# Kernel tuning notes

Measured on AMD Instinct MI355X. Metric: run time of the kernel, lower is better.

Reference implementation:

```python
import jax, jax.numpy as jnp
import numpy as np

ACT_SCALE = 1.0 / 12.0
BATCH = 2_097_152
HIDDEN = 32


def _xavier(key, shape):
    fan_out, fan_in = shape
    std = (2.0 / (fan_in + fan_out)) ** 0.5
    return jax.random.normal(key, shape, dtype=jnp.float32) * std


def setup_inputs() -> dict:
    key = jax.random.key(0)
    ks = jax.random.split(key, 12)
    return {
        "eps_flat": jax.random.normal(ks[0], (BATCH, 3), dtype=jnp.float32) * 0.1,
        "B_first_w": _xavier(ks[1], (HIDDEN, 2)),
        "B_first_b": jax.random.normal(ks[2], (HIDDEN,), dtype=jnp.float32) * 0.05,
        "raw_A_0": jax.random.normal(ks[3], (HIDDEN, HIDDEN), dtype=jnp.float32) * 0.1,
        "raw_A_1": jax.random.normal(ks[4], (HIDDEN, HIDDEN), dtype=jnp.float32) * 0.1,
        "Bs_w_0": _xavier(ks[5], (HIDDEN, 2)),
        "Bs_b_0": jax.random.normal(ks[6], (HIDDEN,), dtype=jnp.float32) * 0.05,
        "Bs_w_1": _xavier(ks[7], (HIDDEN, 2)),
        "Bs_b_1": jax.random.normal(ks[8], (HIDDEN,), dtype=jnp.float32) * 0.05,
        "raw_A_out": jax.random.normal(ks[9], (1, HIDDEN), dtype=jnp.float32) * 0.1,
        "B_out_w": _xavier(ks[10], (1, 2)),
        "B_out_b": jax.random.normal(ks[11], (1,), dtype=jnp.float32) * 0.05,
    }


def reference(eps_flat, B_first_w, B_first_b, raw_A_0, raw_A_1,
              Bs_w_0, Bs_b_0, Bs_w_1, Bs_b_1, raw_A_out, B_out_w, B_out_b):
    sp = jax.nn.softplus

    def forward_W(z0):
        # z0: (n, 2) -> W: (n, 1). Dropout p=0 -> identity.
        z = sp(z0 @ B_first_w.T + B_first_b)
        for rawA, Bw, Bb in ((raw_A_0, Bs_w_0, Bs_b_0), (raw_A_1, Bs_w_1, Bs_b_1)):
            z = ACT_SCALE * sp(z @ sp(rawA).T) ** 2 + sp(z0 @ Bw.T + Bb)
        return z @ sp(raw_A_out).T + z0 @ B_out_w.T + B_out_b

    e11, e22, e12 = eps_flat[:, 0], eps_flat[:, 1], eps_flat[:, 2]
    I1 = e11 + e22
    I2 = e11 ** 2 + 2.0 * e12 ** 2 + e22 ** 2
    z0 = jnp.stack([I1, I2], axis=-1)  # (B, 2)

    W_sum = lambda z: forward_W(z).sum()
    grads = jax.grad(W_sum)(z0)                       # (B, 2) per-sample dW/dz0
    z0_ref = jnp.zeros((1, 2), dtype=eps_flat.dtype)
    dWdI1_ref = jax.grad(W_sum)(z0_ref)[0, 0]         # scalar reference correction

    dW_dI1 = grads[:, 0] - dWdI1_ref
    dW_dI2 = grads[:, 1]
    s11 = dW_dI1 + 2.0 * e11 * dW_dI2
    s22 = dW_dI1 + 2.0 * e22 * dW_dI2
    s12 = 2.0 * e12 * dW_dI2
    return jnp.stack([s11, s22, s12], axis=-1)
```

## Files before the change

kernel.cpp:

```cpp
#include <hip/hip_runtime.h>

typedef __attribute__((ext_vector_type(8)))  short s8b;
typedef __attribute__((ext_vector_type(16))) float f32x16;
typedef __attribute__((ext_vector_type(4)))  uint  uint4v;
typedef __attribute__((ext_vector_type(2)))  float float2v;
typedef __attribute__((ext_vector_type(4)))  float float4v;
typedef uint __attribute__((may_alias)) uint_ma;

static constexpr int   kBatch    = 2097152;
static constexpr float kActScale = 1.0f / 12.0f;
static constexpr float kAct2     = 1.0f / 6.0f;

__device__ float g_tab[40];
__device__ __attribute__((aligned(16))) ushort g_wt[4][2][2][64][8];

__device__ __forceinline__ float rcp_f(float x) { return __fdividef(1.0f, x); }
__device__ __forceinline__ float sp_only(float x) {
    float e = __expf(-fabsf(x));
    return fmaxf(x, 0.0f) + __logf(1.0f + e);
}
__device__ __forceinline__ float sig_only(float x) {
    float e = __expf(-fabsf(x));
    float r = rcp_f(1.0f + e);
    return (x >= 0.0f) ? r : e * r;
}
__device__ __forceinline__ float sp_sig(float x, float& sig) {
    float e  = __expf(-fabsf(x));
    float oe = 1.0f + e;
    float r  = rcp_f(oe);
    sig = (x >= 0.0f) ? r : e * r;
    return fmaxf(x, 0.0f) + __logf(oe);
}

__device__ __forceinline__ float log1p_e(float e) {
    return e * fmaf(e, fmaf(e, fmaf(e, fmaf(e, 0.03215845f, -0.13606275f),
                                    0.28947478f), -0.49190896f), 0.99949556f);
}
__device__ __forceinline__ float rcp12(float u) {
    float r = fmaf(u, -0.5f, 1.4571068f);
    r = r * fmaf(-u, r, 2.0f);
    r = r * fmaf(-u, r, 2.0f);
    return r;
}
__device__ __forceinline__ float sp_sig_p(float x, float& sig) {
    float e = __expf(-fabsf(x));
    float r = rcp12(1.0f + e);
    sig = (x >= 0.0f) ? r : e * r;
    return fmaxf(x, 0.0f) + log1p_e(e);
}
__device__ __forceinline__ float sp_sig_pos(float x, float& sig) {
    float e = __expf(-x);
    sig = rcp12(1.0f + e);
    return x + log1p_e(e);
}
__device__ __forceinline__ float sig_only_p(float x) {
    float e = __expf(-fabsf(x));
    float r = rcp12(1.0f + e);
    return (x >= 0.0f) ? r : e * r;
}

__device__ __forceinline__ uint  bf16u(float x) {
    uint u = __float_as_uint(x);
    return (u + 0x7FFFu + ((u >> 16) & 1u)) >> 16;
}
__device__ __forceinline__ float bf16f(uint h) { return __uint_as_float(h << 16); }
__device__ __forceinline__ uint cvt_pk_bf16(float lo, float hi) {
    uint r;
    asm("v_cvt_pk_bf16_f32 %0, %1, %2" : "=v"(r) : "v"(lo), "v"(hi));
    return r;
}
__device__ __forceinline__ void pswap(uint& a, uint& b) {
    asm("v_permlane32_swap_b32 %0, %1" : "+v"(a), "+v"(b));
}

__global__ __launch_bounds__(256) void icnn_prep(
    const float* __restrict__ rawA0, const float* __restrict__ rawA1,
    const float* __restrict__ rawAout,
    const float* __restrict__ W1,  const float* __restrict__ b1,
    const float* __restrict__ Wc0, const float* __restrict__ bc0,
    const float* __restrict__ Wc1, const float* __restrict__ bc1,
    const float* __restrict__ wout)
{
    __shared__ float sA0[1024], sA1[1024], sAout[32];
    const int t = threadIdx.x;
    for (int k = t; k < 1024; k += 256) sA0[k] = sp_only(rawA0[k]);
    for (int k = t; k < 1024; k += 256) sA1[k] = sp_only(rawA1[k]);
    if (t < 32) { float v = sp_only(rawAout[t]); sAout[t] = v; g_tab[t] = v; }
    __syncthreads();

    for (int k = t; k < 8192; k += 256) {
        int m = k >> 11, r = k & 2047;
        int hl = r >> 10, c = (r >> 9) & 1, l = (r >> 3) & 63, b = r & 7;
        int row = l & 31, j = 16 * c + 8 * (l >> 5) + b;
        float v;
        if      (m == 0) v = sA0[row * 32 + j];
        else if (m == 1) v = sA1[row * 32 + j];
        else if (m == 2) v = sA1[j * 32 + row];
        else             v = sA0[j * 32 + row];
        uint hi = bf16u(v);
        g_wt[m][hl][c][l][b] = (ushort)(hl == 0 ? hi : bf16u(v - bf16f(hi)));
    }

    if (t < 32) {
        const int i = t;
        float sa, sc0v;
        float zi = sp_sig(b1[i], sa);
        float u = 0.0f;
        for (int j = 0; j < 32; j++) u = fmaf(sA0[i * 32 + j], __shfl(zi, j, 64), u);
        float su; float t0 = sp_sig(u, su);
        float d0 = kAct2 * t0 * su;
        float spc = sp_sig(bc0[i], sc0v);
        float zn = fmaf(kActScale * t0, t0, spc);
        float u1 = 0.0f;
        for (int j = 0; j < 32; j++) u1 = fmaf(sA1[i * 32 + j], __shfl(zn, j, 64), u1);
        float su1; float t1 = sp_sig(u1, su1);
        float d1 = sAout[i] * kAct2 * t1 * su1;
        float contrib = Wc1[2 * i] * sAout[i] * sig_only(bc1[i]);
        float g = 0.0f;
        for (int j = 0; j < 32; j++) g = fmaf(sA1[j * 32 + i], __shfl(d1, j, 64), g);
        contrib = fmaf(Wc0[2 * i], g * sc0v, contrib);
        float gu0 = g * d0;
        float ga = 0.0f;
        for (int j = 0; j < 32; j++) ga = fmaf(sA0[j * 32 + i], __shfl(gu0, j, 64), ga);
        ga *= sa;
        contrib = fmaf(W1[2 * i], ga, contrib);
        for (int off = 16; off >= 1; off >>= 1)
            contrib += __shfl_down(contrib, off, 32);
        if (i == 0) g_tab[32] = wout[0] + contrib;
    }
}

__device__ __forceinline__ s8b ldwt(int m, int hl, int c, int lane) {
    const uint_ma* p = (const uint_ma*)&g_wt[m][hl][c][lane][0];
    uint4v q; q.x = p[0]; q.y = p[1]; q.z = p[2]; q.w = p[3];
    return __builtin_bit_cast(s8b, q);
}

#define OFF(e) (((e) & 3) + 8 * ((e) >> 2))

#define SWAPJ(PZ, FA, FB) { \
    uint s0 = PZ[0], s1 = PZ[1], s2 = PZ[2], s3 = PZ[3]; \
    uint s4 = PZ[4], s5 = PZ[5], s6 = PZ[6], s7 = PZ[7]; \
    pswap(s0, s2); pswap(s1, s3); pswap(s4, s6); pswap(s5, s7); \
    uint4v qa, qb; \
    qa.x = s0; qa.y = s1; qa.z = s2; qa.w = s3; \
    qb.x = s4; qb.y = s5; qb.z = s6; qb.w = s7; \
    FA = __builtin_bit_cast(s8b, qa); FB = __builtin_bit_cast(s8b, qb); }

#define MM(m, BA, BB, ACC) { \
    ACC = __builtin_amdgcn_mfma_f32_32x32x16_bf16(ldwt(m, 0, 0, lane), BA, ACC, 0, 0, 0); \
    ACC = __builtin_amdgcn_mfma_f32_32x32x16_bf16(ldwt(m, 0, 1, lane), BB, ACC, 0, 0, 0); \
    ACC = __builtin_amdgcn_mfma_f32_32x32x16_bf16(ldwt(m, 1, 0, lane), BA, ACC, 0, 0, 0); \
    ACC = __builtin_amdgcn_mfma_f32_32x32x16_bf16(ldwt(m, 1, 1, lane), BB, ACC, 0, 0, 0); }

__global__ __launch_bounds__(256) void icnn_main(
    const float* __restrict__ eps,
    const float* __restrict__ W1,  const float* __restrict__ b1,
    const float* __restrict__ Wc0, const float* __restrict__ bc0,
    const float* __restrict__ Wc1, const float* __restrict__ bc1,
    const float* __restrict__ wout,
    float* __restrict__ out)
{
    __shared__ uint carr[4][2][544];
    const int tid  = threadIdx.x;
    const int lane = tid & 63, wib = tid >> 6;
    const bool hb_ = lane >= 32;
    const int  hB  = hb_ ? 1 : 0;
    const int  rowl = lane & 31;
    const long rowg = ((long)blockIdx.x * 4 + wib) * 32 + rowl;
    uint* __restrict__ ca = &carr[wib][0][0];
    uint* __restrict__ cc = &carr[wib][1][0];

    const float e11 = eps[rowg * 3 + 0];
    const float e22 = eps[rowg * 3 + 1];
    const float e12 = eps[rowg * 3 + 2];
    const float x1 = e11 + e22;
    const float x2 = e11 * e11 + 2.0f * e12 * e12 + e22 * e22;

    const float wout0 = wout[0], wout1 = wout[1];
    const float cref  = g_tab[32];
    const char* W1c  = (const char*)W1;
    const char* b1c  = (const char*)b1;
    const char* Wc0c = (const char*)Wc0;
    const char* bc0c = (const char*)bc0;
    const char* Wc1c = (const char*)Wc1;
    const char* bc1c = (const char*)bc1;
    const char* aoc  = (const char*)&g_tab[0];

    float g0p = 0.0f, gqp = 0.0f;

    uint zf[2][4];
    #pragma unroll
    for (int c = 0; c < 2; ++c)
    #pragma unroll
    for (int s = 0; s < 4; ++s) {
        const float4v w4 = *(const float4v*)(W1c + 64 * hB + 128 * c + 16 * s);
        const float2v b2 = *(const float2v*)(b1c + 32 * hB + 64 * c + 8 * s);
        float a0 = fmaf(w4.x, x1, fmaf(w4.y, x2, b2.x));
        float a1 = fmaf(w4.z, x1, fmaf(w4.w, x2, b2.y));
        float s0, s1;
        float z0 = sp_sig_p(a0, s0);
        float z1 = sp_sig_p(a1, s1);
        zf[c][s] = cvt_pk_bf16(z0, z1);
        ca[rowl * 17 + 8 * c + 4 * hB + s] = cvt_pk_bf16(s0, s1);
    }
    uint4v zq0, zq1;
    zq0.x = zf[0][0]; zq0.y = zf[0][1]; zq0.z = zf[0][2]; zq0.w = zf[0][3];
    zq1.x = zf[1][0]; zq1.y = zf[1][1]; zq1.z = zf[1][2]; zq1.w = zf[1][3];
    s8b fA = __builtin_bit_cast(s8b, zq0);
    s8b fB = __builtin_bit_cast(s8b, zq1);

    f32x16 acc = {};
    MM(0, fA, fB, acc)

    uint pd0[8], pz[8];
    #pragma unroll
    for (int q = 0; q < 8; ++q) {
        const int e = 2 * q, off = OFF(e);
        const float4v wc = *(const float4v*)(Wc0c + 32 * hB + 8 * off);
        const float2v bc = *(const float2v*)(bc0c + 16 * hB + 4 * off);
        float su;  float t  = sp_sig_pos(acc[e], su);
        float su2; float t2 = sp_sig_pos(acc[e + 1], su2);
        float c0a = fmaf(wc.x, x1, fmaf(wc.y, x2, bc.x));
        float c0b = fmaf(wc.z, x1, fmaf(wc.w, x2, bc.y));
        float sc0, sc1;
        float spc0 = sp_sig_p(c0a, sc0);
        float spc1 = sp_sig_p(c0b, sc1);
        cc[rowl * 17 + 2 * hB + (off >> 1)] = cvt_pk_bf16(sc0, sc1);
        pd0[q] = cvt_pk_bf16(kAct2 * t * su, kAct2 * t2 * su2);
        pz[q]  = cvt_pk_bf16(fmaf(kActScale * t, t, spc0),
                             fmaf(kActScale * t2, t2, spc1));
    }
    SWAPJ(pz, fA, fB)

    f32x16 acc1 = {};
    MM(1, fA, fB, acc1)

    uint pdd[8];
    #pragma unroll
    for (int q = 0; q < 8; ++q) {
        const int e = 2 * q, off = OFF(e);
        const float4v wc = *(const float4v*)(Wc1c + 32 * hB + 8 * off);
        const float2v bc = *(const float2v*)(bc1c + 16 * hB + 4 * off);
        const float2v ao = *(const float2v*)(aoc  + 16 * hB + 4 * off);
        float c1a = fmaf(wc.x, x1, fmaf(wc.y, x2, bc.x));
        float c1b = fmaf(wc.z, x1, fmaf(wc.w, x2, bc.y));
        float wA = ao.x * sig_only_p(c1a);
        float wB = ao.y * sig_only_p(c1b);
        g0p = fmaf(wc.x, wA, g0p); gqp = fmaf(wc.y, wA, gqp);
        g0p = fmaf(wc.z, wB, g0p); gqp = fmaf(wc.w, wB, gqp);
        float su;  float t  = sp_sig_pos(acc1[e], su);
        float su2; float t2 = sp_sig_pos(acc1[e + 1], su2);
        pdd[q] = cvt_pk_bf16(ao.x * kAct2 * t * su, ao.y * kAct2 * t2 * su2);
    }
    SWAPJ(pdd, fA, fB)

    f32x16 acc2 = {};
    MM(2, fA, fB, acc2)

    uint pgg[8];
    #pragma unroll
    for (int q = 0; q < 8; ++q) {
        const int e = 2 * q, off = OFF(e);
        const float4v wc = *(const float4v*)(Wc0c + 32 * hB + 8 * off);
        uint pk = cc[rowl * 17 + 2 * hB + (off >> 1)];
        float tA = acc2[e]     * bf16f(pk & 0xFFFFu);
        float tB = acc2[e + 1] * bf16f(pk >> 16);
        g0p = fmaf(wc.x, tA, g0p); gqp = fmaf(wc.y, tA, gqp);
        g0p = fmaf(wc.z, tB, g0p); gqp = fmaf(wc.w, tB, gqp);
        pgg[q] = cvt_pk_bf16(acc2[e] * bf16f(pd0[q] & 0xFFFFu),
                             acc2[e + 1] * bf16f(pd0[q] >> 16));
    }
    SWAPJ(pgg, fA, fB)

    f32x16 acc3 = {};
    MM(3, fA, fB, acc3)

    #pragma unroll
    for (int q = 0; q < 8; ++q) {
        const int e = 2 * q, off = OFF(e);
        const float4v w4 = *(const float4v*)(W1c + 32 * hB + 8 * off);
        uint pk = ca[rowl * 17 + 2 * hB + (off >> 1)];
        float gA = acc3[e]     * bf16f(pk & 0xFFFFu);
        float gB = acc3[e + 1] * bf16f(pk >> 16);
        g0p = fmaf(w4.x, gA, g0p); gqp = fmaf(w4.y, gA, gqp);
        g0p = fmaf(w4.z, gB, g0p); gqp = fmaf(w4.w, gB, gqp);
    }

    uint ga_ = __float_as_uint(g0p), gb_ = ga_;
    pswap(ga_, gb_);
    float g0o = __uint_as_float(hb_ ? ga_ : gb_);
    uint qa_ = __float_as_uint(gqp), qb_ = qa_;
    pswap(qa_, qb_);
    float gqo = __uint_as_float(hb_ ? qa_ : qb_);

    float g0f = wout0 + g0p + g0o;
    float gqf = wout1 + gqp + gqo;
    const float dI1 = g0f - cref;
    const float dI2 = gqf;
    if (!hb_) {
        out[rowg * 3 + 0] = fmaf(2.0f * e11, dI2, dI1);
        out[rowg * 3 + 1] = fmaf(2.0f * e22, dI2, dI1);
        out[rowg * 3 + 2] = 2.0f * e12 * dI2;
    }
}

extern "C" void kernel_launch(void* const* d_in, const int* in_sizes, int n_in,
                              void* d_out, int out_size, void* d_ws, size_t ws_size,
                              hipStream_t stream)
{
    (void)in_sizes; (void)n_in; (void)out_size; (void)d_ws; (void)ws_size;
    const float* eps    = (const float*)d_in[0];
    const float* W1     = (const float*)d_in[1];
    const float* b1     = (const float*)d_in[2];
    const float* rawA0  = (const float*)d_in[3];
    const float* rawA1  = (const float*)d_in[4];
    const float* Wc0    = (const float*)d_in[5];
    const float* bc0    = (const float*)d_in[6];
    const float* Wc1    = (const float*)d_in[7];
    const float* bc1    = (const float*)d_in[8];
    const float* rawAout= (const float*)d_in[9];
    const float* wout   = (const float*)d_in[10];
    float* out = (float*)d_out;

    icnn_prep<<<1, 256, 0, stream>>>(rawA0, rawA1, rawAout, W1, b1, Wc0, bc0, Wc1, bc1, wout);
    icnn_main<<<kBatch / 128, 256, 0, stream>>>(eps, W1, b1, Wc0, bc0, Wc1, bc1, wout, out);
}
```

Baseline: 185.5 us.

## Compute input-layer pre-activations with MFMA and keep sigmoids in registers

The three 2-input affine projections (first layer and both skip connections) are now computed with bf16 hi/lo split MFMA ops. Inputs x1, x2 and a constant 1 are packed as the B operand, and per-unit weights and biases are packed into a new global table built by the prep kernel. Because these results come out in the accumulator layout, the sigmoid values for the first layer and skip 0 stay in registers, and the shared-memory scratch arrays and their stores and loads are removed. This trades scalar FMAs, per-lane weight loads and LDS traffic for three extra MFMAs plus bf16 split precision on the projections.

```diff
diff --git a/kernel.cpp b/kernel.cpp
--- a/kernel.cpp
+++ b/kernel.cpp
@@ -13,6 +13,7 @@
 
 __device__ float g_tab[40];
 __device__ __attribute__((aligned(16))) ushort g_wt[4][2][2][64][8];
+__device__ __attribute__((aligned(16))) ushort g_pt[3][64][8];
 
 __device__ __forceinline__ float rcp_f(float x) { return __fdividef(1.0f, x); }
 __device__ __forceinline__ float sp_only(float x) {
@@ -99,6 +100,28 @@
         else             v = sA0[j * 32 + row];
         uint hi = bf16u(v);
         g_wt[m][hl][c][l][b] = (ushort)(hl == 0 ? hi : bf16u(v - bf16f(hi)));
+    }
+
+    for (int k = t; k < 1536; k += 256) {
+        int m = k >> 9, r = k & 511, l = r >> 3, b = r & 7;
+        int unit = l & 31, half = l >> 5;
+        ushort v = 0;
+        if (half == 0) {
+            const float* Wm = (m == 0) ? W1 : ((m == 1) ? Wc0 : Wc1);
+            const float* Bm = (m == 0) ? b1 : ((m == 1) ? bc0 : bc1);
+            float w1 = Wm[2 * unit], w2 = Wm[2 * unit + 1], bb = Bm[unit];
+            uint h;
+            switch (b) {
+                case 0: v = (ushort)bf16u(w1); break;
+                case 1: h = bf16u(w1); v = (ushort)bf16u(w1 - bf16f(h)); break;
+                case 2: v = (ushort)bf16u(w2); break;
+                case 3: h = bf16u(w2); v = (ushort)bf16u(w2 - bf16f(h)); break;
+                case 4: v = (ushort)bf16u(bb); break;
+                case 5: h = bf16u(bb); v = (ushort)bf16u(bb - bf16f(h)); break;
+                default: v = 0;
+            }
+        }
+        g_pt[m][l][b] = v;
     }
 
     if (t < 32) {
@@ -135,6 +158,11 @@
     uint4v q; q.x = p[0]; q.y = p[1]; q.z = p[2]; q.w = p[3];
     return __builtin_bit_cast(s8b, q);
 }
+__device__ __forceinline__ s8b ldpt(int m, int lane) {
+    const uint_ma* p = (const uint_ma*)&g_pt[m][lane][0];
+    uint4v q; q.x = p[0]; q.y = p[1]; q.z = p[2]; q.w = p[3];
+    return __builtin_bit_cast(s8b, q);
+}
 
 #define OFF(e) (((e) & 3) + 8 * ((e) >> 2))
 
@@ -161,15 +189,12 @@
     const float* __restrict__ wout,
     float* __restrict__ out)
 {
-    __shared__ uint carr[4][2][544];
     const int tid  = threadIdx.x;
     const int lane = tid & 63, wib = tid >> 6;
     const bool hb_ = lane >= 32;
     const int  hB  = hb_ ? 1 : 0;
     const int  rowl = lane & 31;
     const long rowg = ((long)blockIdx.x * 4 + wib) * 32 + rowl;
-    uint* __restrict__ ca = &carr[wib][0][0];
-    uint* __restrict__ cc = &carr[wib][1][0];
 
     const float e11 = eps[rowg * 3 + 0];
     const float e22 = eps[rowg * 3 + 1];
@@ -180,53 +205,53 @@
     const float wout0 = wout[0], wout1 = wout[1];
     const float cref  = g_tab[32];
     const char* W1c  = (const char*)W1;
-    const char* b1c  = (const char*)b1;
     const char* Wc0c = (const char*)Wc0;
-    const char* bc0c = (const char*)bc0;
     const char* Wc1c = (const char*)Wc1;
-    const char* bc1c = (const char*)bc1;
     const char* aoc  = (const char*)&g_tab[0];
 
     float g0p = 0.0f, gqp = 0.0f;
 
-    uint zf[2][4];
-    #pragma unroll
-    for (int c = 0; c < 2; ++c)
-    #pragma unroll
-    for (int s = 0; s < 4; ++s) {
-        const float4v w4 = *(const float4v*)(W1c + 64 * hB + 128 * c + 16 * s);
-        const float2v b2 = *(const float2v*)(b1c + 32 * hB + 64 * c + 8 * s);
-        float a0 = fmaf(w4.x, x1, fmaf(w4.y, x2, b2.x));
-        float a1 = fmaf(w4.z, x1, fmaf(w4.w, x2, b2.y));
+    uint x1h = bf16u(x1);
+    uint x1l = bf16u(x1 - bf16f(x1h));
+    uint x2h = bf16u(x2);
+    uint x2l = bf16u(x2 - bf16f(x2h));
+    uint4v bq;
+    bq.x = hb_ ? 0u : (x1h | (x1l << 16));
+    bq.y = hb_ ? 0u : (x2h | (x2l << 16));
+    bq.z = hb_ ? 0u : 0x3F803F80u;
+    bq.w = 0u;
+    s8b bx = __builtin_bit_cast(s8b, bq);
+    f32x16 zzz = {};
+    f32x16 pa  = __builtin_amdgcn_mfma_f32_32x32x16_bf16(ldpt(0, lane), bx, zzz, 0, 0, 0);
+    f32x16 pc0 = __builtin_amdgcn_mfma_f32_32x32x16_bf16(ldpt(1, lane), bx, zzz, 0, 0, 0);
+    f32x16 pc1 = __builtin_amdgcn_mfma_f32_32x32x16_bf16(ldpt(2, lane), bx, zzz, 0, 0, 0);
+
+    uint pz[8], psa[8];
+    #pragma unroll
+    for (int q = 0; q < 8; ++q) {
+        const int e = 2 * q;
         float s0, s1;
-        float z0 = sp_sig_p(a0, s0);
-        float z1 = sp_sig_p(a1, s1);
-        zf[c][s] = cvt_pk_bf16(z0, z1);
-        ca[rowl * 17 + 8 * c + 4 * hB + s] = cvt_pk_bf16(s0, s1);
-    }
-    uint4v zq0, zq1;
-    zq0.x = zf[0][0]; zq0.y = zf[0][1]; zq0.z = zf[0][2]; zq0.w = zf[0][3];
-    zq1.x = zf[1][0]; zq1.y = zf[1][1]; zq1.z = zf[1][2]; zq1.w = zf[1][3];
-    s8b fA = __builtin_bit_cast(s8b, zq0);
-    s8b fB = __builtin_bit_cast(s8b, zq1);
+        float z0 = sp_sig_p(pa[e],     s0);
+        float z1 = sp_sig_p(pa[e + 1], s1);
+        pz[q]  = cvt_pk_bf16(z0, z1);
+        psa[q] = cvt_pk_bf16(s0, s1);
+    }
+    s8b fA, fB;
+    SWAPJ(pz, fA, fB)
 
     f32x16 acc = {};
     MM(0, fA, fB, acc)
 
-    uint pd0[8], pz[8];
-    #pragma unroll
-    for (int q = 0; q < 8; ++q) {
-        const int e = 2 * q, off = OFF(e);
-        const float4v wc = *(const float4v*)(Wc0c + 32 * hB + 8 * off);
-        const float2v bc = *(const float2v*)(bc0c + 16 * hB + 4 * off);
+    uint pd0[8], psc[8];
+    #pragma unroll
+    for (int q = 0; q < 8; ++q) {
+        const int e = 2 * q;
         float su;  float t  = sp_sig_pos(acc[e], su);
         float su2; float t2 = sp_sig_pos(acc[e + 1], su2);
-        float c0a = fmaf(wc.x, x1, fmaf(wc.y, x2, bc.x));
-        float c0b = fmaf(wc.z, x1, fmaf(wc.w, x2, bc.y));
         float sc0, sc1;
-        float spc0 = sp_sig_p(c0a, sc0);
-        float spc1 = sp_sig_p(c0b, sc1);
-        cc[rowl * 17 + 2 * hB + (off >> 1)] = cvt_pk_bf16(sc0, sc1);
+        float spc0 = sp_sig_p(pc0[e],     sc0);
+        float spc1 = sp_sig_p(pc0[e + 1], sc1);
+        psc[q] = cvt_pk_bf16(sc0, sc1);
         pd0[q] = cvt_pk_bf16(kAct2 * t * su, kAct2 * t2 * su2);
         pz[q]  = cvt_pk_bf16(fmaf(kActScale * t, t, spc0),
                              fmaf(kActScale * t2, t2, spc1));
@@ -241,12 +266,9 @@
     for (int q = 0; q < 8; ++q) {
         const int e = 2 * q, off = OFF(e);
         const float4v wc = *(const float4v*)(Wc1c + 32 * hB + 8 * off);
-        const float2v bc = *(const float2v*)(bc1c + 16 * hB + 4 * off);
         const float2v ao = *(const float2v*)(aoc  + 16 * hB + 4 * off);
-        float c1a = fmaf(wc.x, x1, fmaf(wc.y, x2, bc.x));
-        float c1b = fmaf(wc.z, x1, fmaf(wc.w, x2, bc.y));
-        float wA = ao.x * sig_only_p(c1a);
-        float wB = ao.y * sig_only_p(c1b);
+        float wA = ao.x * sig_only_p(pc1[e]);
+        float wB = ao.y * sig_only_p(pc1[e + 1]);
         g0p = fmaf(wc.x, wA, g0p); gqp = fmaf(wc.y, wA, gqp);
         g0p = fmaf(wc.z, wB, g0p); gqp = fmaf(wc.w, wB, gqp);
         float su;  float t  = sp_sig_pos(acc1[e], su);
@@ -263,9 +285,8 @@
     for (int q = 0; q < 8; ++q) {
         const int e = 2 * q, off = OFF(e);
         const float4v wc = *(const float4v*)(Wc0c + 32 * hB + 8 * off);
-        uint pk = cc[rowl * 17 + 2 * hB + (off >> 1)];
-        float tA = acc2[e]     * bf16f(pk & 0xFFFFu);
-        float tB = acc2[e + 1] * bf16f(pk >> 16);
+        float tA = acc2[e]     * bf16f(psc[q] & 0xFFFFu);
+        float tB = acc2[e + 1] * bf16f(psc[q] >> 16);
         g0p = fmaf(wc.x, tA, g0p); gqp = fmaf(wc.y, tA, gqp);
         g0p = fmaf(wc.z, tB, g0p); gqp = fmaf(wc.w, tB, gqp);
         pgg[q] = cvt_pk_bf16(acc2[e] * bf16f(pd0[q] & 0xFFFFu),
@@ -280,9 +301,8 @@
     for (int q = 0; q < 8; ++q) {
         const int e = 2 * q, off = OFF(e);
         const float4v w4 = *(const float4v*)(W1c + 32 * hB + 8 * off);
-        uint pk = ca[rowl * 17 + 2 * hB + (off >> 1)];
-        float gA = acc3[e]     * bf16f(pk & 0xFFFFu);
-        float gB = acc3[e + 1] * bf16f(pk >> 16);
+        float gA = acc3[e]     * bf16f(psa[q] & 0xFFFFu);
+        float gB = acc3[e + 1] * bf16f(psa[q] >> 16);
         g0p = fmaf(w4.x, gA, g0p); gqp = fmaf(w4.y, gA, gqp);
         g0p = fmaf(w4.z, gB, g0p); gqp = fmaf(w4.w, gB, gqp);
     }
```

Result: slower. 192.0 us (+3.5%).
